# Optimization experiments

Hardware: AMD Instinct MI355X
Metric: run time of the kernel (lower is better)

The kernel has to match this reference:

```python
import jax, jax.numpy as jnp
import numpy as np

N, E, B, H = 20000, 100000, 512, 64
IN_CH, EDGE_DIM, OUT_CH = 16, 8, 1


def setup_inputs() -> dict:
    key = jax.random.key(0)
    ks = jax.random.split(key, 20)
    rn = lambda k, shp, s=0.1: (jax.random.normal(k, shp, jnp.float32) * s)
    return {
        'x': rn(ks[0], (N, IN_CH), 1.0),
        'edge_index': jax.random.randint(ks[1], (2, E), 0, N),
        'edge_attr': rn(ks[2], (E, EDGE_DIM), 1.0),
        'batch': jnp.sort(jax.random.randint(ks[3], (N,), 0, B)),
        'lin0_w': rn(ks[4], (IN_CH, H)), 'lin0_b': jnp.zeros((H,), jnp.float32),
        'nn1_w': rn(ks[5], (EDGE_DIM, 128)), 'nn1_b': jnp.zeros((128,), jnp.float32),
        'nn2_w': rn(ks[6], (128, H * H), 0.02), 'nn2_b': jnp.zeros((H * H,), jnp.float32),
        'root_w': rn(ks[7], (H, H)), 'root_b': jnp.zeros((H,), jnp.float32),
        'gru_wih': rn(ks[8], (H, 3 * H)), 'gru_whh': rn(ks[9], (H, 3 * H)),
        'gru_bih': jnp.zeros((3 * H,), jnp.float32), 'gru_bhh': jnp.zeros((3 * H,), jnp.float32),
        'lstm_wih': rn(ks[10], (2 * H, 4 * H)), 'lstm_whh': rn(ks[11], (H, 4 * H)),
        'lstm_bih': jnp.zeros((4 * H,), jnp.float32), 'lstm_bhh': jnp.zeros((4 * H,), jnp.float32),
        'lin1_w': rn(ks[12], (2 * H, H)), 'lin1_b': jnp.zeros((H,), jnp.float32),
        'lin2_w': rn(ks[13], (H, OUT_CH)), 'lin2_b': jnp.zeros((OUT_CH,), jnp.float32),
    }


def reference(x, edge_index, edge_attr, batch, lin0_w, lin0_b, nn1_w, nn1_b,
              nn2_w, nn2_b, root_w, root_b, gru_wih, gru_whh, gru_bih, gru_bhh,
              lstm_wih, lstm_whh, lstm_bih, lstm_bhh, lin1_w, lin1_b, lin2_w, lin2_b):
    src, dst = edge_index[0], edge_index[1]
    # edge network weights (shared across the 3 message-passing steps)
    ew = jax.nn.relu(edge_attr @ nn1_w + nn1_b) @ nn2_w + nn2_b  # [E, H*H]
    ew = ew.reshape(E, H, H)
    deg = jnp.maximum(jax.ops.segment_sum(jnp.ones((E,), x.dtype), dst, N), 1.0)

    out = jax.nn.relu(x @ lin0_w + lin0_b)  # [N, H]
    h = out
    for _ in range(3):
        # NNConv: gather src feats, per-edge matvec, scatter-mean to dst, + root linear
        msg = jnp.einsum('ei,eio->eo', out[src], ew)                  # [E, H]
        agg = jax.ops.segment_sum(msg, dst, N) / deg[:, None]          # [N, H]
        m = jax.nn.relu(agg + out @ root_w + root_b)
        # GRU cell (torch gate order r, z, n)
        gi = m @ gru_wih + gru_bih
        gh = h @ gru_whh + gru_bhh
        r = jax.nn.sigmoid(gi[:, :H] + gh[:, :H])
        z = jax.nn.sigmoid(gi[:, H:2 * H] + gh[:, H:2 * H])
        n = jnp.tanh(gi[:, 2 * H:] + r * gh[:, 2 * H:])
        h = (1.0 - z) * n + z * h
        out = h

    # Set2Set pooling, 3 processing steps (torch LSTM gate order i, f, g, o)
    q_star = jnp.zeros((B, 2 * H), x.dtype)
    hh = jnp.zeros((B, H), x.dtype)
    cc = jnp.zeros((B, H), x.dtype)
    for _ in range(3):
        g = q_star @ lstm_wih + hh @ lstm_whh + lstm_bih + lstm_bhh    # [B, 4H]
        i_g = jax.nn.sigmoid(g[:, :H])
        f_g = jax.nn.sigmoid(g[:, H:2 * H])
        g_g = jnp.tanh(g[:, 2 * H:3 * H])
        o_g = jax.nn.sigmoid(g[:, 3 * H:])
        cc = f_g * cc + i_g * g_g
        hh = o_g * jnp.tanh(cc)
        q = hh                                                          # [B, H]
        e = jnp.sum(out * q[batch], axis=-1)                            # [N]
        e_max = jax.ops.segment_max(e, batch, B)
        a = jnp.exp(e - e_max[batch])
        a = a / jax.ops.segment_sum(a, batch, B)[batch]
        rvec = jax.ops.segment_sum(a[:, None] * out, batch, B)          # [B, H]
        q_star = jnp.concatenate([q, rvec], axis=-1)

    y = jax.nn.relu(q_star @ lin1_w + lin1_b) @ lin2_w + lin2_b         # [B, 1]
    return y
```

## Files before the change

kernel.cpp:

```cpp
#include <hip/hip_runtime.h>
#include <hip/hip_bf16.h>
#include <hip/hip_fp16.h>
#include <cstddef>
#include <cstdint>

#define N_NODES 20000
#define N_EDGES 100000
#define N_BATCH 512

#define EPB 96
#define TS 6
#define ECAP 100032

typedef __attribute__((ext_vector_type(8))) short ushort8_t;
typedef __attribute__((ext_vector_type(8))) _Float16 f16x8;
typedef __attribute__((ext_vector_type(4))) float f32x4;

union F16x8U { f16x8 v; unsigned int u[4]; };

__device__ __forceinline__ float sigmoidf_(float x) { return 1.f / (1.f + expf(-x)); }
__device__ __forceinline__ unsigned short f2h(float x) {
    return __half_as_ushort(__float2half(x));
}
__device__ __forceinline__ float h2f(unsigned short s) {
    return __half2float(__ushort_as_half(s));
}

#define LIN0_BLOCKS 5000
#define BSW_BLOCKS 258
#define CNT_BLOCKS 391

__global__ __launch_bounds__(256) void prep1_kernel(
        const float* __restrict__ x, const float* __restrict__ l0w, const float* __restrict__ l0b,
        const float* __restrict__ w2, const float* __restrict__ b2,
        const int* __restrict__ ei,
        float* __restrict__ out, unsigned short* __restrict__ bsw,
        int* __restrict__ cnt, int E) {
    int bid = blockIdx.x, tid = threadIdx.x;
    if (bid < LIN0_BLOCKS) {
        int idx = bid * 256 + tid;
        int n = idx >> 6, j = idx & 63;
        float acc = l0b[j];
#pragma unroll
        for (int i = 0; i < 16; i++) acc += x[n * 16 + i] * l0w[i * 64 + j];
        out[idx] = fmaxf(acc, 0.f);
    } else if (bid < LIN0_BLOCKS + BSW_BLOCKS) {
        int idx = (bid - LIN0_BLOCKS) * 256 + tid;
        if (idx < 66048) {
            int l = idx & 63, oc = (idx >> 6) & 3, ks = idx >> 8;
            int o = oc * 16 + (l & 15);
            int kap0 = ks * 32 + 8 * (l >> 4);
#pragma unroll
            for (int j = 0; j < 8; ++j) {
                int kap = kap0 + j;
                int k = kap >> 6, i = kap & 63;
                float v = (k < 128) ? w2[(size_t)k * 4096 + i * 64 + o] : b2[i * 64 + o];
                bsw[(size_t)idx * 8 + j] = f2h(v);
            }
        }
    } else {
        int e = (bid - LIN0_BLOCKS - BSW_BLOCKS) * 256 + tid;
        if (e < E) atomicAdd(&cnt[ei[E + e]], 1);
    }
}

__global__ __launch_bounds__(1024) void scan_kernel(const int* __restrict__ cnt,
                                                    int* __restrict__ cstart,
                                                    int* __restrict__ cursor,
                                                    float* __restrict__ degf, int n) {
    __shared__ int part[1024];
    int t = threadIdx.x;
    int base = t * 20;
    int loc[20];
    int s = 0;
#pragma unroll
    for (int i = 0; i < 20; ++i) {
        int idx = base + i;
        int c = (idx < n) ? cnt[idx] : 0;
        loc[i] = s;
        s += c;
    }
    part[t] = s;
    __syncthreads();
    for (int off = 1; off < 1024; off <<= 1) {
        int v = (t >= off) ? part[t - off] : 0;
        __syncthreads();
        part[t] += v;
        __syncthreads();
    }
    int tb = part[t] - s;
#pragma unroll
    for (int i = 0; i < 20; ++i) {
        int idx = base + i;
        if (idx < n) {
            int b0 = tb + loc[i];
            cstart[idx] = b0;
            cursor[idx] = b0;
            degf[idx] = (float)cnt[idx];
        }
    }
}

__global__ void place_kernel(const int* __restrict__ ei, const float* __restrict__ ea,
                             int* __restrict__ cursor,
                             int* __restrict__ src_s, float* __restrict__ ea_s, int E) {
    int e = blockIdx.x * 256 + threadIdx.x;
    if (e < E) {
        int dst = ei[E + e];
        int slot = atomicAdd(&cursor[dst], 1);
        src_s[slot] = ei[e];
        const float4* s = (const float4*)(ea + (size_t)e * 8);
        float4 a = s[0], b = s[1];
        float4* d = (float4*)(ea_s + (size_t)slot * 8);
        d[0] = a; d[1] = b;
    }
}

template<int HUPIPE>
__global__ __launch_bounds__(256, 2) void msg_mfma(const float* __restrict__ out,
                                                   const float* __restrict__ ea_s,
                                                   const float* __restrict__ w1g,
                                                   const float* __restrict__ b1g,
                                                   const unsigned short* __restrict__ bsw,
                                                   const int* __restrict__ src_s,
                                                   unsigned short* __restrict__ msgp, int E) {
    __shared__ __align__(16) unsigned short hs16[128 * EPB];
    __shared__ __align__(16) float w1l[8 * 128];
    __shared__ __align__(16) float b1l[128];
    const int tid = threadIdx.x;
    const int w = tid >> 6, l = tid & 63;
    const int e0 = blockIdx.x * EPB;
    const int r16 = l & 15, q = l >> 4;

    {
        f32x4 v = *(const f32x4*)&w1g[tid * 4];
        *(f32x4*)&w1l[tid * 4] = v;
        if (tid < 32) *(f32x4*)&b1l[tid * 4] = *(const f32x4*)&b1g[tid * 4];
    }

    f16x8 sfrag[TS][2];
#pragma unroll
    for (int t = 0; t < TS; ++t) {
        int e = e0 + t * 16 + r16;
        int src = (e < E) ? src_s[e] : 0;
        const f32x4* p = (const f32x4*)(out + (size_t)src * 64);
#pragma unroll
        for (int st = 0; st < 2; ++st) {
            f16x8 f = {};
            if (e < E) {
                f32x4 a = p[st * 8 + q * 2], b = p[st * 8 + q * 2 + 1];
#pragma unroll
                for (int j = 0; j < 4; ++j) { f[j] = (_Float16)a[j]; f[4 + j] = (_Float16)b[j]; }
            }
            sfrag[t][st] = f;
        }
    }

    __syncthreads();

    if (tid < 192) {
        int ep = tid >> 1;
        int koff = (tid & 1) * 64;
        int e = e0 + ep;
        bool v = e < E;
        float ear[8];
        const float* earow = ea_s + (size_t)(v ? e : 0) * 8;
#pragma unroll
        for (int i = 0; i < 8; ++i) ear[i] = earow[i];
#pragma unroll
        for (int kv = 0; kv < 16; ++kv) {
            int k = koff + kv * 4;
            f32x4 a = *(const f32x4*)&b1l[k];
#pragma unroll
            for (int i = 0; i < 8; ++i) {
                f32x4 wv = *(const f32x4*)&w1l[i * 128 + k];
                a += ear[i] * wv;
            }
#pragma unroll
            for (int jj = 0; jj < 4; ++jj)
                hs16[(k + jj) * EPB + ep] = v ? f2h(fmaxf(a[jj], 0.f)) : (unsigned short)0;
        }
    }

    const f16x8* bp = (const f16x8*)bsw;
    f16x8 bfA[8], bfB[8];
#pragma unroll
    for (int i = 0; i < 8; ++i) bfA[i] = bp[((w * 8 + i) << 6) + l];

    __syncthreads();

    f32x4 acc[TS][4] = {};

#define MSG_BODY(HUEXPR, BF)                                                   \
    {                                                                          \
        _Pragma("unroll")                                                      \
        for (int t = 0; t < TS; ++t) {                                         \
            unsigned int hu = (HUEXPR);                                        \
            _Pragma("unroll")                                                  \
            for (int st = 0; st < 2; ++st) {                                   \
                F16x8U s_, a_;                                                 \
                s_.v = sfrag[t][st];                                           \
                asm("v_pk_mul_f16 %0, %1, %2 op_sel:[0,0] op_sel_hi:[0,1]"     \
                    : "=v"(a_.u[0]) : "v"(hu), "v"(s_.u[0]));                  \
                asm("v_pk_mul_f16 %0, %1, %2 op_sel:[0,0] op_sel_hi:[0,1]"     \
                    : "=v"(a_.u[1]) : "v"(hu), "v"(s_.u[1]));                  \
                asm("v_pk_mul_f16 %0, %1, %2 op_sel:[0,0] op_sel_hi:[0,1]"     \
                    : "=v"(a_.u[2]) : "v"(hu), "v"(s_.u[2]));                  \
                asm("v_pk_mul_f16 %0, %1, %2 op_sel:[0,0] op_sel_hi:[0,1]"     \
                    : "=v"(a_.u[3]) : "v"(hu), "v"(s_.u[3]));                  \
                _Pragma("unroll")                                              \
                for (int oc = 0; oc < 4; ++oc)                                 \
                    acc[t][oc] = __builtin_amdgcn_mfma_f32_16x16x32_f16(       \
                        a_.v, BF[st * 4 + oc], acc[t][oc], 0, 0, 0);           \
            }                                                                  \
        }                                                                      \
    }

    if constexpr (!HUPIPE) {
#pragma unroll 1
        for (int kk = 0; kk < 16; ++kk) {
            int k1 = w + kk * 8;
            int k2 = k1 + 4;
#pragma unroll
            for (int i = 0; i < 8; ++i) bfB[i] = bp[((k2 * 8 + i) << 6) + l];
            MSG_BODY(hs16[k1 * EPB + t * 16 + r16], bfA);
            if (kk < 15) {
                int k3 = k1 + 8;
#pragma unroll
                for (int i = 0; i < 8; ++i) bfA[i] = bp[((k3 * 8 + i) << 6) + l];
            }
            MSG_BODY(hs16[k2 * EPB + t * 16 + r16], bfB);
        }
    } else {
        unsigned int huA[TS], huB[TS];
#pragma unroll
        for (int t = 0; t < TS; ++t) huA[t] = hs16[w * EPB + t * 16 + r16];
#pragma unroll 1
        for (int kk = 0; kk < 16; ++kk) {
            int k1 = w + kk * 8;
            int k2 = k1 + 4;
            int k3 = (kk < 15) ? (k1 + 8) : k1;
#pragma unroll
            for (int i = 0; i < 8; ++i) bfB[i] = bp[((k2 * 8 + i) << 6) + l];
#pragma unroll
            for (int t = 0; t < TS; ++t) huB[t] = hs16[k2 * EPB + t * 16 + r16];
            MSG_BODY(huA[t], bfA);
            if (kk < 15) {
#pragma unroll
                for (int i = 0; i < 8; ++i) bfA[i] = bp[((k3 * 8 + i) << 6) + l];
            }
#pragma unroll
            for (int t = 0; t < TS; ++t) huA[t] = hs16[k3 * EPB + t * 16 + r16];
            MSG_BODY(huB[t], bfB);
        }
    }
#undef MSG_BODY

    if (w == 0) {
#pragma unroll
        for (int i = 0; i < 8; ++i) bfA[i] = bp[((128 * 8 + i) << 6) + l];
#pragma unroll
        for (int t = 0; t < TS; ++t)
#pragma unroll
            for (int st = 0; st < 2; ++st)
#pragma unroll
                for (int oc = 0; oc < 4; ++oc)
                    acc[t][oc] = __builtin_amdgcn_mfma_f32_16x16x32_f16(
                        sfrag[t][st], bfA[st * 4 + oc], acc[t][oc], 0, 0, 0);
    }

    unsigned short* slab = msgp + (size_t)w * ECAP * 64;
#pragma unroll
    for (int t = 0; t < TS; ++t) {
#pragma unroll
        for (int r = 0; r < 4; ++r) {
            int e = e0 + t * 16 + q * 4 + r;
            if (e < E) {
                unsigned short* row = slab + (size_t)e * 64 + r16;
                row[0]  = f2h(acc[t][0][r]);
                row[16] = f2h(acc[t][1][r]);
                row[32] = f2h(acc[t][2][r]);
                row[48] = f2h(acc[t][3][r]);
            }
        }
    }
}

__global__ __launch_bounds__(256) void gru_kernel(float* __restrict__ out,
                                                  const unsigned short* __restrict__ msgp,
                                                  const int* __restrict__ cstart,
                                                  const int* __restrict__ cnt,
                                                  const float* __restrict__ deg,
                                                  const float* __restrict__ root_w,
                                                  const float* __restrict__ root_b,
                                                  const float* __restrict__ wih,
                                                  const float* __restrict__ whh,
                                                  const float* __restrict__ bih,
                                                  const float* __restrict__ bhh) {
    int w = threadIdx.x >> 6, j = threadIdx.x & 63;
    int n = blockIdx.x * 4 + w;
    __shared__ float s_o[4][64];
    __shared__ float s_m[4][64];
    s_o[w][j] = out[(size_t)n * 64 + j];
    __syncthreads();

    float msum = 0.f;
    {
        int base = cstart[n], c = cnt[n];
        for (int s2 = 0; s2 < c; ++s2) {
            size_t slot = (size_t)(base + s2) * 64 + j;
            float a0 = h2f(msgp[slot]);
            float a1 = h2f(msgp[(size_t)ECAP * 64 + slot]);
            float a2 = h2f(msgp[2 * (size_t)ECAP * 64 + slot]);
            float a3 = h2f(msgp[3 * (size_t)ECAP * 64 + slot]);
            msum += (a0 + a1) + (a2 + a3);
        }
    }
    float d = deg[n]; if (d < 1.f) d = 1.f;
    float mv = msum / d + root_b[j];
#pragma unroll 8
    for (int i = 0; i < 64; i++) mv += s_o[w][i] * root_w[i * 64 + j];
    mv = fmaxf(mv, 0.f);
    s_m[w][j] = mv;
    __syncthreads();
    float gi_r = bih[j], gi_z = bih[64 + j], gi_n = bih[128 + j];
    float gh_r = bhh[j], gh_z = bhh[64 + j], gh_n = bhh[128 + j];
#pragma unroll 4
    for (int i = 0; i < 64; i++) {
        float m = s_m[w][i], hv = s_o[w][i];
        gi_r += m * wih[i * 192 + j];
        gi_z += m * wih[i * 192 + 64 + j];
        gi_n += m * wih[i * 192 + 128 + j];
        gh_r += hv * whh[i * 192 + j];
        gh_z += hv * whh[i * 192 + 64 + j];
        gh_n += hv * whh[i * 192 + 128 + j];
    }
    float r = sigmoidf_(gi_r + gh_r);
    float z = sigmoidf_(gi_z + gh_z);
    float nn = tanhf(gi_n + r * gh_n);
    float hnew = (1.f - z) * nn + z * s_o[w][j];
    out[(size_t)n * 64 + j] = hnew;
}

__global__ __launch_bounds__(256) void s2s_final(const float* __restrict__ out,
                                                 const int* __restrict__ batch,
                                                 const float* __restrict__ wih,
                                                 const float* __restrict__ whh,
                                                 const float* __restrict__ bih,
                                                 const float* __restrict__ bhh,
                                                 const float* __restrict__ w1,
                                                 const float* __restrict__ b1,
                                                 const float* __restrict__ w2,
                                                 const float* __restrict__ b2,
                                                 float* __restrict__ y, int N) {
    int b = blockIdx.x;
    int tid = threadIdx.x;
    int gate = tid >> 6, j = tid & 63;
    __shared__ float s_qs[128];
    __shared__ float s_g[4][64];
    __shared__ float s_h[64];
    __shared__ float s_c[64];
    __shared__ int s_lo, s_hi;
    __shared__ float s_red[4];
    __shared__ float s_rv[4][64];

    if (tid < 128) s_qs[tid] = 0.f;
    if (gate == 2) s_h[j] = 0.f;
    if (gate == 3) s_c[j] = 0.f;
    if (tid == 0) {
        int lo = 0, hi = N;
        while (lo < hi) { int mid = (lo + hi) >> 1; if (batch[mid] < b) lo = mid + 1; else hi = mid; }
        s_lo = lo;
        int lo2 = lo, hi2 = N;
        while (lo2 < hi2) { int mid = (lo2 + hi2) >> 1; if (batch[mid] < b + 1) lo2 = mid + 1; else hi2 = mid; }
        s_hi = lo2;
    }
    __syncthreads();

    for (int it = 0; it < 3; ++it) {
        float g = bih[gate * 64 + j] + bhh[gate * 64 + j];
#pragma unroll 4
        for (int i = 0; i < 128; ++i) g += s_qs[i] * wih[i * 256 + gate * 64 + j];
#pragma unroll 4
        for (int i = 0; i < 64; ++i) g += s_h[i] * whh[i * 256 + gate * 64 + j];
        s_g[gate][j] = g;
        __syncthreads();
        if (gate == 0) {
            float c = sigmoidf_(s_g[1][j]) * s_c[j] + sigmoidf_(s_g[0][j]) * tanhf(s_g[2][j]);
            float h = sigmoidf_(s_g[3][j]) * tanhf(c);
            s_c[j] = c;
            s_h[j] = h;
            s_qs[j] = h;
        }
        __syncthreads();

        int lo = s_lo, hi = s_hi;
        float wmax = -3.402823e38f;
        for (int n = lo + gate; n < hi; n += 4) {
            float p = out[(size_t)n * 64 + j] * s_h[j];
#pragma unroll
            for (int d = 32; d >= 1; d >>= 1) p += __shfl_xor(p, d);
            wmax = fmaxf(wmax, p);
        }
        if (j == 0) s_red[gate] = wmax;
        __syncthreads();
        float m = fmaxf(fmaxf(s_red[0], s_red[1]), fmaxf(s_red[2], s_red[3]));
        __syncthreads();
        float ssum = 0.f, rv = 0.f;
        for (int n = lo + gate; n < hi; n += 4) {
            float xv = out[(size_t)n * 64 + j];
            float p = xv * s_h[j];
#pragma unroll
            for (int d = 32; d >= 1; d >>= 1) p += __shfl_xor(p, d);
            float a = expf(p - m);
            ssum += a;
            rv += a * xv;
        }
        if (j == 0) s_red[gate] = ssum;
        s_rv[gate][j] = rv;
        __syncthreads();
        if (gate == 0) {
            float S = s_red[0] + s_red[1] + s_red[2] + s_red[3];
            float r = s_rv[0][j] + s_rv[1][j] + s_rv[2][j] + s_rv[3][j];
            s_qs[64 + j] = (S > 0.f) ? r / S : 0.f;
        }
        __syncthreads();
    }

    if (gate == 0) {
        float tv = b1[j];
#pragma unroll 4
        for (int i = 0; i < 128; ++i) tv += s_qs[i] * w1[i * 64 + j];
        tv = fmaxf(tv, 0.f);
        float p = tv * w2[j];
#pragma unroll
        for (int d = 32; d >= 1; d >>= 1) p += __shfl_xor(p, d);
        if (j == 0) y[b] = p + b2[0];
    }
}

extern "C" void kernel_launch(void* const* d_in, const int* in_sizes, int n_in,
                              void* d_out, int out_size, void* d_ws, size_t ws_size,
                              hipStream_t stream) {
    const int N = N_NODES, E = N_EDGES, B = N_BATCH;
    const float* x       = (const float*)d_in[0];
    const int*   ei      = (const int*)d_in[1];
    const float* ea      = (const float*)d_in[2];
    const int*   batch   = (const int*)d_in[3];
    const float* lin0_w  = (const float*)d_in[4];
    const float* lin0_b  = (const float*)d_in[5];
    const float* nn1_w   = (const float*)d_in[6];
    const float* nn1_b   = (const float*)d_in[7];
    const float* nn2_w   = (const float*)d_in[8];
    const float* nn2_b   = (const float*)d_in[9];
    const float* root_w  = (const float*)d_in[10];
    const float* root_b  = (const float*)d_in[11];
    const float* gru_wih = (const float*)d_in[12];
    const float* gru_whh = (const float*)d_in[13];
    const float* gru_bih = (const float*)d_in[14];
    const float* gru_bhh = (const float*)d_in[15];
    const float* lstm_wih = (const float*)d_in[16];
    const float* lstm_whh = (const float*)d_in[17];
    const float* lstm_bih = (const float*)d_in[18];
    const float* lstm_bhh = (const float*)d_in[19];
    const float* lin1_w  = (const float*)d_in[20];
    const float* lin1_b  = (const float*)d_in[21];
    const float* lin2_w  = (const float*)d_in[22];
    const float* lin2_b  = (const float*)d_in[23];
    float* y = (float*)d_out;

    char* ws = (char*)d_ws;
    size_t off = 0;
    auto alloc = [&](size_t bytes) { void* p = ws + off; off = (off + bytes + 255) & ~(size_t)255; return p; };
    unsigned short* bsw  = (unsigned short*)alloc((size_t)66048 * 8 * 2);
    unsigned short* msgp = (unsigned short*)alloc((size_t)4 * ECAP * 64 * 2);
    float* ea_s   = (float*)alloc((size_t)ECAP * 8 * 4);
    float* out    = (float*)alloc((size_t)N * 64 * 4);
    float* deg    = (float*)alloc((size_t)N * 4);
    int*   cnt    = (int*)alloc((size_t)N * 4);
    int*   cstart = (int*)alloc((size_t)N * 4);
    int*   cursor = (int*)alloc((size_t)N * 4);
    int*   src_s  = (int*)alloc((size_t)E * 4);

    hipMemsetAsync(cnt, 0, (size_t)N * 4, stream);

    prep1_kernel<<<LIN0_BLOCKS + BSW_BLOCKS + CNT_BLOCKS, 256, 0, stream>>>(
        x, lin0_w, lin0_b, nn2_w, nn2_b, ei, out, bsw, cnt, E);
    scan_kernel<<<1, 1024, 0, stream>>>(cnt, cstart, cursor, deg, N);
    place_kernel<<<(E + 255) / 256, 256, 0, stream>>>(ei, ea, cursor, src_s, ea_s, E);

    msg_mfma<0><<<(E + EPB - 1) / EPB, 256, 0, stream>>>(out, ea_s, nn1_w, nn1_b,
                                                         bsw, src_s, msgp, E);
    gru_kernel<<<N / 4, 256, 0, stream>>>(out, msgp, cstart, cnt, deg, root_w, root_b,
                                          gru_wih, gru_whh, gru_bih, gru_bhh);
    for (int step = 1; step < 3; ++step) {
        msg_mfma<1><<<(E + EPB - 1) / EPB, 256, 0, stream>>>(out, ea_s, nn1_w, nn1_b,
                                                             bsw, src_s, msgp, E);
        gru_kernel<<<N / 4, 256, 0, stream>>>(out, msgp, cstart, cnt, deg, root_w, root_b,
                                              gru_wih, gru_whh, gru_bih, gru_bhh);
    }

    s2s_final<<<B, 256, 0, stream>>>(out, batch, lstm_wih, lstm_whh, lstm_bih, lstm_bhh,
                                     lin1_w, lin1_b, lin2_w, lin2_b, y, N);
}
```

Before: 672.1 us.

## Add 32x32x16 MFMA variant of message kernel with matching weight layout

Adds a second weight swizzle (bsw32) in the prep kernel laid out for 32x32x16 f16 MFMA, and a SHAPE=1 path in msg_mfma that gathers source features into 32-row fragments and accumulates into 32x32 tiles. Steps 2 and 3 use this path, while step 1 keeps the 16x16x32 path. The larger MFMA tiles are meant to raise math throughput per instruction and cut B-fragment reuse overhead. In exchange it adds extra prep work and workspace, uses more accumulator registers, and scatters the output with a different write pattern.

```diff
diff --git a/kernel.cpp b/kernel.cpp
--- a/kernel.cpp
+++ b/kernel.cpp
@@ -15,6 +15,7 @@
 typedef __attribute__((ext_vector_type(8))) short ushort8_t;
 typedef __attribute__((ext_vector_type(8))) _Float16 f16x8;
 typedef __attribute__((ext_vector_type(4))) float f32x4;
+typedef __attribute__((ext_vector_type(16))) float f32x16;
 
 union F16x8U { f16x8 v; unsigned int u[4]; };
 
@@ -28,14 +29,15 @@
 
 #define LIN0_BLOCKS 5000
 #define BSW_BLOCKS 258
+#define BSW32_BLOCKS 258
 #define CNT_BLOCKS 391
 
 __global__ __launch_bounds__(256) void prep1_kernel(
         const float* __restrict__ x, const float* __restrict__ l0w, const float* __restrict__ l0b,
         const float* __restrict__ w2, const float* __restrict__ b2,
         const int* __restrict__ ei,
-        float* __restrict__ out, unsigned short* __restrict__ bsw,
-        int* __restrict__ cnt, int E) {
+        float* __restrict__ out, unsigned short* __restrict__ bsw16,
+        unsigned short* __restrict__ bsw32, int* __restrict__ cnt, int E) {
     int bid = blockIdx.x, tid = threadIdx.x;
     if (bid < LIN0_BLOCKS) {
         int idx = bid * 256 + tid;
@@ -55,11 +57,24 @@
                 int kap = kap0 + j;
                 int k = kap >> 6, i = kap & 63;
                 float v = (k < 128) ? w2[(size_t)k * 4096 + i * 64 + o] : b2[i * 64 + o];
-                bsw[(size_t)idx * 8 + j] = f2h(v);
+                bsw16[(size_t)idx * 8 + j] = f2h(v);
+            }
+        }
+    } else if (bid < LIN0_BLOCKS + BSW_BLOCKS + BSW32_BLOCKS) {
+        int idx = (bid - LIN0_BLOCKS - BSW_BLOCKS) * 256 + tid;
+        if (idx < 66048) {
+            int l = idx & 63, oc = (idx >> 6) & 1, c = (idx >> 7) & 3, k = idx >> 9;
+            int o = oc * 32 + (l & 31);
+            int i0 = c * 16 + 8 * (l >> 5);
+#pragma unroll
+            for (int j = 0; j < 8; ++j) {
+                int i = i0 + j;
+                float v = (k < 128) ? w2[(size_t)k * 4096 + i * 64 + o] : b2[i * 64 + o];
+                bsw32[(size_t)idx * 8 + j] = f2h(v);
             }
         }
     } else {
-        int e = (bid - LIN0_BLOCKS - BSW_BLOCKS) * 256 + tid;
+        int e = (bid - LIN0_BLOCKS - BSW_BLOCKS - BSW32_BLOCKS) * 256 + tid;
         if (e < E) atomicAdd(&cnt[ei[E + e]], 1);
     }
 }
@@ -116,7 +131,7 @@
     }
 }
 
-template<int HUPIPE>
+template<int SHAPE>
 __global__ __launch_bounds__(256, 2) void msg_mfma(const float* __restrict__ out,
                                                    const float* __restrict__ ea_s,
                                                    const float* __restrict__ w1g,
@@ -131,29 +146,12 @@
     const int w = tid >> 6, l = tid & 63;
     const int e0 = blockIdx.x * EPB;
     const int r16 = l & 15, q = l >> 4;
+    const int l31 = l & 31, hi = l >> 5;
 
     {
         f32x4 v = *(const f32x4*)&w1g[tid * 4];
         *(f32x4*)&w1l[tid * 4] = v;
         if (tid < 32) *(f32x4*)&b1l[tid * 4] = *(const f32x4*)&b1g[tid * 4];
-    }
-
-    f16x8 sfrag[TS][2];
-#pragma unroll
-    for (int t = 0; t < TS; ++t) {
-        int e = e0 + t * 16 + r16;
-        int src = (e < E) ? src_s[e] : 0;
-        const f32x4* p = (const f32x4*)(out + (size_t)src * 64);
-#pragma unroll
-        for (int st = 0; st < 2; ++st) {
-            f16x8 f = {};
-            if (e < E) {
-                f32x4 a = p[st * 8 + q * 2], b = p[st * 8 + q * 2 + 1];
-#pragma unroll
-                for (int j = 0; j < 4; ++j) { f[j] = (_Float16)a[j]; f[4 + j] = (_Float16)b[j]; }
-            }
-            sfrag[t][st] = f;
-        }
     }
 
     __syncthreads();
@@ -183,19 +181,39 @@
     }
 
     const f16x8* bp = (const f16x8*)bsw;
-    f16x8 bfA[8], bfB[8];
-#pragma unroll
-    for (int i = 0; i < 8; ++i) bfA[i] = bp[((w * 8 + i) << 6) + l];
-
-    __syncthreads();
-
-    f32x4 acc[TS][4] = {};
-
-#define MSG_BODY(HUEXPR, BF)                                                   \
+
+    if constexpr (SHAPE == 0) {
+        f16x8 sfrag[TS][2];
+#pragma unroll
+        for (int t = 0; t < TS; ++t) {
+            int e = e0 + t * 16 + r16;
+            int src = (e < E) ? src_s[e] : 0;
+            const f32x4* p = (const f32x4*)(out + (size_t)src * 64);
+#pragma unroll
+            for (int st = 0; st < 2; ++st) {
+                f16x8 f = {};
+                if (e < E) {
+                    f32x4 a = p[st * 8 + q * 2], b = p[st * 8 + q * 2 + 1];
+#pragma unroll
+                    for (int j = 0; j < 4; ++j) { f[j] = (_Float16)a[j]; f[4 + j] = (_Float16)b[j]; }
+                }
+                sfrag[t][st] = f;
+            }
+        }
+
+        f16x8 bfA[8], bfB[8];
+#pragma unroll
+        for (int i = 0; i < 8; ++i) bfA[i] = bp[((w * 8 + i) << 6) + l];
+
+        __syncthreads();
+
+        f32x4 acc[TS][4] = {};
+
+#define MSG_BODY16(K, BF)                                                      \
     {                                                                          \
         _Pragma("unroll")                                                      \
         for (int t = 0; t < TS; ++t) {                                         \
-            unsigned int hu = (HUEXPR);                                        \
+            unsigned int hu = hs16[(K) * EPB + t * 16 + r16];                  \
             _Pragma("unroll")                                                  \
             for (int st = 0; st < 2; ++st) {                                   \
                 F16x8U s_, a_;                                                 \
@@ -216,73 +234,143 @@
         }                                                                      \
     }
 
-    if constexpr (!HUPIPE) {
 #pragma unroll 1
         for (int kk = 0; kk < 16; ++kk) {
             int k1 = w + kk * 8;
             int k2 = k1 + 4;
 #pragma unroll
             for (int i = 0; i < 8; ++i) bfB[i] = bp[((k2 * 8 + i) << 6) + l];
-            MSG_BODY(hs16[k1 * EPB + t * 16 + r16], bfA);
+            MSG_BODY16(k1, bfA);
             if (kk < 15) {
                 int k3 = k1 + 8;
 #pragma unroll
                 for (int i = 0; i < 8; ++i) bfA[i] = bp[((k3 * 8 + i) << 6) + l];
             }
-            MSG_BODY(hs16[k2 * EPB + t * 16 + r16], bfB);
+            MSG_BODY16(k2, bfB);
+        }
+#undef MSG_BODY16
+
+        if (w == 0) {
+#pragma unroll
+            for (int i = 0; i < 8; ++i) bfA[i] = bp[((128 * 8 + i) << 6) + l];
+#pragma unroll
+            for (int t = 0; t < TS; ++t)
+#pragma unroll
+                for (int st = 0; st < 2; ++st)
+#pragma unroll
+                    for (int oc = 0; oc < 4; ++oc)
+                        acc[t][oc] = __builtin_amdgcn_mfma_f32_16x16x32_f16(
+                            sfrag[t][st], bfA[st * 4 + oc], acc[t][oc], 0, 0, 0);
+        }
+
+        unsigned short* slab = msgp + (size_t)w * ECAP * 64;
+#pragma unroll
+        for (int t = 0; t < TS; ++t) {
+#pragma unroll
+            for (int r = 0; r < 4; ++r) {
+                int e = e0 + t * 16 + q * 4 + r;
+                if (e < E) {
+                    unsigned short* row = slab + (size_t)e * 64 + r16;
+                    row[0]  = f2h(acc[t][0][r]);
+                    row[16] = f2h(acc[t][1][r]);
+                    row[32] = f2h(acc[t][2][r]);
+                    row[48] = f2h(acc[t][3][r]);
+                }
+            }
         }
     } else {
-        unsigned int huA[TS], huB[TS];
-#pragma unroll
-        for (int t = 0; t < TS; ++t) huA[t] = hs16[w * EPB + t * 16 + r16];
+        f16x8 sfr[3][4];
+#pragma unroll
+        for (int t = 0; t < 3; ++t) {
+            int e = e0 + t * 32 + l31;
+            int src = (e < E) ? src_s[e] : 0;
+            const f32x4* p = (const f32x4*)(out + (size_t)src * 64);
+#pragma unroll
+            for (int c = 0; c < 4; ++c) {
+                f16x8 f = {};
+                if (e < E) {
+                    f32x4 a = p[c * 4 + 2 * hi], b = p[c * 4 + 2 * hi + 1];
+#pragma unroll
+                    for (int j = 0; j < 4; ++j) { f[j] = (_Float16)a[j]; f[4 + j] = (_Float16)b[j]; }
+                }
+                sfr[t][c] = f;
+            }
+        }
+
+        f16x8 bfA[8], bfB[8];
+#pragma unroll
+        for (int i = 0; i < 8; ++i) bfA[i] = bp[((w * 8 + i) << 6) + l];
+
+        __syncthreads();
+
+        f32x16 acc[3][2] = {};
+
+#define MSG_BODY32(K, BF)                                                      \
+    {                                                                          \
+        _Pragma("unroll")                                                      \
+        for (int t = 0; t < 3; ++t) {                                          \
+            unsigned int hu = hs16[(K) * EPB + t * 32 + l31];                  \
+            _Pragma("unroll")                                                  \
+            for (int c = 0; c < 4; ++c) {                                      \
+                F16x8U s_, a_;                                                 \
+                s_.v = sfr[t][c];                                              \
+                asm("v_pk_mul_f16 %0, %1, %2 op_sel:[0,0] op_sel_hi:[0,1]"     \
+                    : "=v"(a_.u[0]) : "v"(hu), "v"(s_.u[0]));                  \
+                asm("v_pk_mul_f16 %0, %1, %2 op_sel:[0,0] op_sel_hi:[0,1]"     \
+                    : "=v"(a_.u[1]) : "v"(hu), "v"(s_.u[1]));                  \
+                asm("v_pk_mul_f16 %0, %1, %2 op_sel:[0,0] op_sel_hi:[0,1]"     \
+                    : "=v"(a_.u[2]) : "v"(hu), "v"(s_.u[2]));                  \
+                asm("v_pk_mul_f16 %0, %1, %2 op_sel:[0,0] op_sel_hi:[0,1]"     \
+                    : "=v"(a_.u[3]) : "v"(hu), "v"(s_.u[3]));                  \
+                acc[t][0] = __builtin_amdgcn_mfma_f32_32x32x16_f16(            \
+                    a_.v, BF[c * 2 + 0], acc[t][0], 0, 0, 0);                  \
+                acc[t][1] = __builtin_amdgcn_mfma_f32_32x32x16_f16(            \
+                    a_.v, BF[c * 2 + 1], acc[t][1], 0, 0, 0);                  \
+            }                                                                  \
+        }                                                                      \
+    }
+
 #pragma unroll 1
         for (int kk = 0; kk < 16; ++kk) {
             int k1 = w + kk * 8;
             int k2 = k1 + 4;
-            int k3 = (kk < 15) ? (k1 + 8) : k1;
 #pragma unroll
             for (int i = 0; i < 8; ++i) bfB[i] = bp[((k2 * 8 + i) << 6) + l];
-#pragma unroll
-            for (int t = 0; t < TS; ++t) huB[t] = hs16[k2 * EPB + t * 16 + r16];
-            MSG_BODY(huA[t], bfA);
+            MSG_BODY32(k1, bfA);
             if (kk < 15) {
+                int k3 = k1 + 8;
 #pragma unroll
                 for (int i = 0; i < 8; ++i) bfA[i] = bp[((k3 * 8 + i) << 6) + l];
             }
-#pragma unroll
-            for (int t = 0; t < TS; ++t) huA[t] = hs16[k3 * EPB + t * 16 + r16];
-            MSG_BODY(huB[t], bfB);
-        }
-    }
-#undef MSG_BODY
-
-    if (w == 0) {
-#pragma unroll
-        for (int i = 0; i < 8; ++i) bfA[i] = bp[((128 * 8 + i) << 6) + l];
-#pragma unroll
-        for (int t = 0; t < TS; ++t)
-#pragma unroll
-            for (int st = 0; st < 2; ++st)
-#pragma unroll
-                for (int oc = 0; oc < 4; ++oc)
-                    acc[t][oc] = __builtin_amdgcn_mfma_f32_16x16x32_f16(
-                        sfrag[t][st], bfA[st * 4 + oc], acc[t][oc], 0, 0, 0);
-    }
-
-    unsigned short* slab = msgp + (size_t)w * ECAP * 64;
-#pragma unroll
-    for (int t = 0; t < TS; ++t) {
-#pragma unroll
-        for (int r = 0; r < 4; ++r) {
-            int e = e0 + t * 16 + q * 4 + r;
-            if (e < E) {
-                unsigned short* row = slab + (size_t)e * 64 + r16;
-                row[0]  = f2h(acc[t][0][r]);
-                row[16] = f2h(acc[t][1][r]);
-                row[32] = f2h(acc[t][2][r]);
-                row[48] = f2h(acc[t][3][r]);
-            }
-        }
+            MSG_BODY32(k2, bfB);
+        }
+#undef MSG_BODY32
+
+        if (w == 0) {
+#pragma unroll
+            for (int i = 0; i < 8; ++i) bfA[i] = bp[((128 * 8 + i) << 6) + l];
+#pragma unroll
+            for (int t = 0; t < 3; ++t)
+#pragma unroll
+                for (int c = 0; c < 4; ++c) {
+                    acc[t][0] = __builtin_amdgcn_mfma_f32_32x32x16_f16(
+                        sfr[t][c], bfA[c * 2 + 0], acc[t][0], 0, 0, 0);
+                    acc[t][1] = __builtin_amdgcn_mfma_f32_32x32x16_f16(
+                        sfr[t][c], bfA[c * 2 + 1], acc[t][1], 0, 0, 0);
+                }
+        }
+
+        unsigned short* slab = msgp + (size_t)w * ECAP * 64;
+#pragma unroll
+        for (int t = 0; t < 3; ++t)
+#pragma unroll
+            for (int oc = 0; oc < 2; ++oc)
+#pragma unroll
+                for (int r = 0; r < 16; ++r) {
+                    int e = e0 + t * 32 + (r & 3) + 8 * (r >> 2) + 4 * hi;
+                    if (e < E)
+                        slab[(size_t)e * 64 + oc * 32 + l31] = f2h(acc[t][oc][r]);
+                }
     }
 }
 
@@ -472,8 +560,9 @@
     char* ws = (char*)d_ws;
     size_t off = 0;
     auto alloc = [&](size_t bytes) { void* p = ws + off; off = (off + bytes + 255) & ~(size_t)255; return p; };
-    unsigned short* bsw  = (unsigned short*)alloc((size_t)66048 * 8 * 2);
-    unsigned short* msgp = (unsigned short*)alloc((size_t)4 * ECAP * 64 * 2);
+    unsigned short* bsw16 = (unsigned short*)alloc((size_t)66048 * 8 * 2);
+    unsigned short* bsw32 = (unsigned short*)alloc((size_t)66048 * 8 * 2);
+    unsigned short* msgp  = (unsigned short*)alloc((size_t)4 * ECAP * 64 * 2);
     float* ea_s   = (float*)alloc((size_t)ECAP * 8 * 4);
     float* out    = (float*)alloc((size_t)N * 64 * 4);
     float* deg    = (float*)alloc((size_t)N * 4);
@@ -484,18 +573,18 @@
 
     hipMemsetAsync(cnt, 0, (size_t)N * 4, stream);
 
-    prep1_kernel<<<LIN0_BLOCKS + BSW_BLOCKS + CNT_BLOCKS, 256, 0, stream>>>(
-        x, lin0_w, lin0_b, nn2_w, nn2_b, ei, out, bsw, cnt, E);
+    prep1_kernel<<<LIN0_BLOCKS + BSW_BLOCKS + BSW32_BLOCKS + CNT_BLOCKS, 256, 0, stream>>>(
+        x, lin0_w, lin0_b, nn2_w, nn2_b, ei, out, bsw16, bsw32, cnt, E);
     scan_kernel<<<1, 1024, 0, stream>>>(cnt, cstart, cursor, deg, N);
     place_kernel<<<(E + 255) / 256, 256, 0, stream>>>(ei, ea, cursor, src_s, ea_s, E);
 
     msg_mfma<0><<<(E + EPB - 1) / EPB, 256, 0, stream>>>(out, ea_s, nn1_w, nn1_b,
-                                                         bsw, src_s, msgp, E);
+                                                         bsw16, src_s, msgp, E);
     gru_kernel<<<N / 4, 256, 0, stream>>>(out, msgp, cstart, cnt, deg, root_w, root_b,
                                           gru_wih, gru_whh, gru_bih, gru_bhh);
     for (int step = 1; step < 3; ++step) {
         msg_mfma<1><<<(E + EPB - 1) / EPB, 256, 0, stream>>>(out, ea_s, nn1_w, nn1_b,
-                                                             bsw, src_s, msgp, E);
+                                                             bsw32, src_s, msgp, E);
         gru_kernel<<<N / 4, 256, 0, stream>>>(out, msgp, cstart, cnt, deg, root_w, root_b,
                                               gru_wih, gru_whh, gru_bih, gru_bhh);
     }
```

Result: slower. 694.0 us (+3.3%).
